# Performance work log

Measured on AMD Instinct MI355X. Metric: run time of the kernel, lower is better.

The kernel has to match this reference:

```python
import jax, jax.numpy as jnp
import numpy as np

C = 128
N = 4096
B = 4
NEG = -9e15


def _bn(x, g, b):
    # training-mode BatchNorm1d over (batch, N); x: [B, C, N]
    mean = x.mean(axis=(0, 2), keepdims=True)
    var = x.var(axis=(0, 2), keepdims=True)  # biased, like torch BN
    xh = (x - mean) * jax.lax.rsqrt(var + 1e-5)
    return xh * g[None, :, None] + b[None, :, None]


def _sa(x, mask2, wqk, wv, bv, wt, bt, g, b):
    # x: [B, C, N]; wqk: [C//4, C] (q and k share weights)
    xq = jnp.einsum('oc,bcn->bno', wqk, x)          # [B, N, C/4]
    xk = jnp.einsum('oc,bcm->bom', wqk, x)          # [B, C/4, N]
    energy = jnp.einsum('bno,bom->bnm', xq, xk)     # [B, N, N]
    energy = jnp.where(mask2, energy, NEG)
    attn = jax.nn.softmax(energy, axis=-1)
    # offset-attention: column-wise L1 renormalization
    attn = attn / (1e-9 + attn.sum(axis=1, keepdims=True))
    xv = jnp.einsum('oc,bcn->bon', wv, x) + bv[None, :, None]
    x_r = jnp.einsum('bcn,bnm->bcm', xv, attn)      # [B, C, N]
    x_r = jax.nn.relu(_bn(jnp.einsum('oc,bcn->bon', wt, x - x_r) + bt[None, :, None], g, b))
    return x + x_r


def setup_inputs() -> dict:
    key = jax.random.key(0)
    ks = jax.random.split(key, 12)
    s = 1.0 / np.sqrt(C)
    return {
        'x': jax.random.normal(ks[0], (B, C, N), jnp.float32),
        'mask': jax.random.randint(ks[1], (B, N), 0, 2, jnp.int32),
        'w1': jax.random.normal(ks[2], (C, C), jnp.float32) * s,
        'g1': jnp.ones((C,), jnp.float32),
        'b1': jnp.zeros((C,), jnp.float32),
        'w2': jax.random.normal(ks[3], (C, C), jnp.float32) * s,
        'g2': jnp.ones((C,), jnp.float32),
        'b2': jnp.zeros((C,), jnp.float32),
        'wqk': jax.random.normal(ks[4], (4, C // 4, C), jnp.float32) * s,
        'wv': jax.random.normal(ks[5], (4, C, C), jnp.float32) * s,
        'bv': jax.random.normal(ks[6], (4, C), jnp.float32) * 0.01,
        'wt': jax.random.normal(ks[7], (4, C, C), jnp.float32) * s,
        'bt': jax.random.normal(ks[8], (4, C), jnp.float32) * 0.01,
        'sg': jnp.ones((4, C), jnp.float32),
        'sb': jnp.zeros((4, C), jnp.float32),
    }


def reference(x, mask, w1, g1, b1, w2, g2, b2, wqk, wv, bv, wt, bt, sg, sb):
    m = mask.astype(bool)
    mask2 = m[:, :, None] & m[:, None, :]           # [B, N, N]
    x = jax.nn.relu(_bn(jnp.einsum('oc,bcn->bon', w1, x), g1, b1))
    x = jax.nn.relu(_bn(jnp.einsum('oc,bcn->bon', w2, x), g2, b2))
    outs = []
    h = x
    for i in range(4):
        h = _sa(h, mask2, wqk[i], wv[i], bv[i], wt[i], bt[i], sg[i], sb[i])
        outs.append(h)
    return jnp.concatenate(outs, axis=1)            # [B, 4C, N]
```

## Files before the change

### kernel.cpp

```cpp
#include <hip/hip_runtime.h>
#include <hip/hip_fp16.h>

constexpr int C = 128;
constexpr int N = 4096;
constexpr int B = 4;

typedef _Float16 f16x8 __attribute__((ext_vector_type(8)));
typedef _Float16 f16x4 __attribute__((ext_vector_type(4)));
typedef float    f32x4 __attribute__((ext_vector_type(4)));

__global__ __launch_bounds__(256) void k_wcvt(const float* __restrict__ w1,
                                              const float* __restrict__ w2,
                                              const float* __restrict__ wv,
                                              const float* __restrict__ wt,
                                              const float* __restrict__ wqk,
                                              _Float16* __restrict__ WF) {
  const int g = blockIdx.x * 256 + threadIdx.x;
  const float* src; int off;
  if (g < 4096)       { src = w1;  off = g; }
  else if (g < 8192)  { src = w2;  off = g - 4096; }
  else if (g < 24576) { src = wv;  off = g - 8192; }
  else if (g < 40960) { src = wt;  off = g - 24576; }
  else                { src = wqk; off = g - 40960; }
  const float4 v = ((const float4*)src)[off];
  f16x4 h = {(_Float16)v.x, (_Float16)v.y, (_Float16)v.z, (_Float16)v.w};
  *(f16x4*)&WF[(size_t)g * 4] = h;
}

__global__ __launch_bounds__(1024) void k_mask(const int* __restrict__ mask,
                                               int* __restrict__ psum,
                                               int* __restrict__ nvb) {
  const int b = blockIdx.x, tid = threadIdx.x;
  __shared__ int wsum[16];
  const int4 mv = *(const int4*)&mask[b * N + tid * 4];
  const int m0 = (mv.x != 0), m1 = (mv.y != 0), m2 = (mv.z != 0), m3 = (mv.w != 0);
  const int s0 = m0, s1 = s0 + m1, s2 = s1 + m2, s3 = s2 + m3;
  const int lane = tid & 63, w = tid >> 6;
  int sc = s3;
#pragma unroll
  for (int o = 1; o < 64; o <<= 1) {
    const int v = __shfl_up(sc, o, 64);
    if (lane >= o) sc += v;
  }
  if (lane == 63) wsum[w] = sc;
  __syncthreads();
  if (tid < 16) {
    int v = wsum[tid];
#pragma unroll
    for (int o = 1; o < 16; o <<= 1) {
      const int u = __shfl_up(v, o, 64);
      if (tid >= o) v += u;
    }
    wsum[tid] = v;
  }
  __syncthreads();
  const int excl = ((w > 0) ? wsum[w - 1] : 0) + sc - s3;
  int4 pv;
  pv.x = excl; pv.y = excl + s0; pv.z = excl + s1; pv.w = excl + s2;
  *(int4*)&psum[b * N + tid * 4] = pv;
  if (tid == 0) nvb[b] = wsum[15];
}

template<bool BIAS, bool STAT, bool F16IN>
__global__ __launch_bounds__(512) void k_gwm(const _Float16* __restrict__ WF,
                                             const void* __restrict__ Xv,
                                             const float* __restrict__ bias,
                                             _Float16* __restrict__ Y,
                                             float* __restrict__ bnpart) {
  __shared__ _Float16 XT[64 * 136];
  __shared__ float statP[4][64], statQ[4][64];
  const int tid = threadIdx.x;
  const int n0 = blockIdx.x * 64, oh = blockIdx.y, b = blockIdx.z;
  if constexpr (F16IN) {
    const _Float16* Xb = (const _Float16*)Xv + (size_t)(b * C) * N + n0;
#pragma unroll
    for (int i = 0; i < 2; i++) {
      const int idx = tid + i * 512;
      const int c = idx >> 3, q = idx & 7;
      const f16x8 v = *(const f16x8*)&Xb[(size_t)c * N + q * 8];
#pragma unroll
      for (int e = 0; e < 8; e++) XT[(q * 8 + e) * 136 + c] = v[e];
    }
  } else {
    const float* Xb = (const float*)Xv + (size_t)(b * C) * N + n0;
#pragma unroll
    for (int i = 0; i < 4; i++) {
      const int idx = tid + i * 512;
      const int c = idx >> 4, q = idx & 15;
      const float4 v = *(const float4*)&Xb[(size_t)c * N + q * 4];
      XT[(q * 4 + 0) * 136 + c] = (_Float16)v.x;
      XT[(q * 4 + 1) * 136 + c] = (_Float16)v.y;
      XT[(q * 4 + 2) * 136 + c] = (_Float16)v.z;
      XT[(q * 4 + 3) * 136 + c] = (_Float16)v.w;
    }
  }
  __syncthreads();
  const int w = tid >> 6, lane = tid & 63, quad = lane >> 4, lr = lane & 15;
  const int nt = w & 3, og = w >> 2;
  const int ob[2] = {oh * 64 + og * 16, oh * 64 + (og + 2) * 16};
  f16x8 aW[2][4];
#pragma unroll
  for (int t = 0; t < 2; t++)
#pragma unroll
    for (int kc = 0; kc < 4; kc++)
      aW[t][kc] = *(const f16x8*)&WF[(size_t)(ob[t] + lr) * 128 + kc * 32 + quad * 8];
  f32x4 acc[2];
  acc[0] = (f32x4){0.f, 0.f, 0.f, 0.f};
  acc[1] = (f32x4){0.f, 0.f, 0.f, 0.f};
#pragma unroll
  for (int kc = 0; kc < 4; kc++) {
    const f16x8 bf = *(const f16x8*)&XT[(nt * 16 + lr) * 136 + kc * 32 + quad * 8];
    acc[0] = __builtin_amdgcn_mfma_f32_16x16x32_f16(aW[0][kc], bf, acc[0], 0, 0, 0);
    acc[1] = __builtin_amdgcn_mfma_f32_16x16x32_f16(aW[1][kc], bf, acc[1], 0, 0, 0);
  }
#pragma unroll
  for (int t = 0; t < 2; t++) {
#pragma unroll
    for (int r = 0; r < 4; r++) {
      const int o = ob[t] + quad * 4 + r;
      const float val = acc[t][r] + (BIAS ? bias[o] : 0.f);
      Y[(size_t)(b * C + o) * N + n0 + nt * 16 + lr] = (_Float16)val;
      if (STAT) {
        float s = val, q = val * val;
        s += __shfl_xor(s, 1, 64); q += __shfl_xor(q, 1, 64);
        s += __shfl_xor(s, 2, 64); q += __shfl_xor(q, 2, 64);
        s += __shfl_xor(s, 4, 64); q += __shfl_xor(q, 4, 64);
        s += __shfl_xor(s, 8, 64); q += __shfl_xor(q, 8, 64);
        if (lr == 0) { statP[nt][o - oh * 64] = s; statQ[nt][o - oh * 64] = q; }
      }
    }
  }
  if (STAT) {
    __syncthreads();
    if (tid < 64) {
      const int o = oh * 64 + tid;
      const float s = statP[0][tid] + statP[1][tid] + statP[2][tid] + statP[3][tid];
      const float q = statQ[0][tid] + statQ[1][tid] + statQ[2][tid] + statQ[3][tid];
      const int part = blockIdx.x * 4 + b;
      bnpart[o * 512 + part] = s;
      bnpart[o * 512 + 256 + part] = q;
    }
  }
}

__global__ __launch_bounds__(256) void k_qv(const _Float16* __restrict__ WFv,
                                            const _Float16* __restrict__ WFqk,
                                            const float* __restrict__ X,
                                            const float* __restrict__ bv,
                                            const int* __restrict__ mask,
                                            const int* __restrict__ psum,
                                            _Float16* __restrict__ XVc,
                                            _Float16* __restrict__ QT,
                                            _Float16* __restrict__ QTc,
                                            float* __restrict__ xvp) {
  __shared__ _Float16 XT[32 * 136];
  __shared__ float SP[2][128];
  const int tid = threadIdx.x;
  const int n0 = blockIdx.x * 32, b = blockIdx.y;
  const float* Xb = X + (size_t)(b * C) * N + n0;
#pragma unroll
  for (int i = 0; i < 4; i++) {
    const int idx = tid + i * 256;
    const int c = idx >> 3, q = idx & 7;
    const float4 v = *(const float4*)&Xb[(size_t)c * N + q * 4];
    XT[(q * 4 + 0) * 136 + c] = (_Float16)v.x;
    XT[(q * 4 + 1) * 136 + c] = (_Float16)v.y;
    XT[(q * 4 + 2) * 136 + c] = (_Float16)v.z;
    XT[(q * 4 + 3) * 136 + c] = (_Float16)v.w;
  }
  __syncthreads();
  const int w = tid >> 6, lane = tid & 63, quad = lane >> 4, lr = lane & 15;
  const int nt = w & 1, og = w >> 1;
  const int n = n0 + nt * 16 + lr;
  const int vld = mask[b * N + n] != 0;
  const int jc = psum[b * N + n];
  f32x4 acc[5];
  const _Float16* Aptr[5];
  int otl[5];
#pragma unroll
  for (int j = 0; j < 5; j++) {
    acc[j] = (f32x4){0.f, 0.f, 0.f, 0.f};
    const int ot = og + 2 * j;
    otl[j] = ot;
    Aptr[j] = (ot < 8) ? (WFv + (size_t)(ot * 16 + lr) * 128)
                       : (WFqk + (size_t)((ot - 8) * 16 + lr) * 128);
  }
#pragma unroll
  for (int kc = 0; kc < 4; kc++) {
    const f16x8 bf = *(const f16x8*)&XT[(nt * 16 + lr) * 136 + kc * 32 + quad * 8];
#pragma unroll
    for (int j = 0; j < 5; j++) {
      const f16x8 a = *(const f16x8*)&Aptr[j][kc * 32 + quad * 8];
      acc[j] = __builtin_amdgcn_mfma_f32_16x16x32_f16(a, bf, acc[j], 0, 0, 0);
    }
  }
#pragma unroll
  for (int j = 0; j < 5; j++) {
    const int ot = otl[j];
    if (ot < 8) {
      float v[4];
#pragma unroll
      for (int r = 0; r < 4; r++) v[r] = acc[j][r] + bv[ot * 16 + quad * 4 + r];
      if (vld) {
#pragma unroll
        for (int r = 0; r < 4; r++)
          XVc[(size_t)(b * C + ot * 16 + quad * 4 + r) * N + jc] = (_Float16)v[r];
      }
      float s[4];
#pragma unroll
      for (int r = 0; r < 4; r++) s[r] = vld ? 0.f : v[r];
#pragma unroll
      for (int o = 1; o <= 8; o <<= 1) {
#pragma unroll
        for (int r = 0; r < 4; r++) s[r] += __shfl_xor(s[r], o, 64);
      }
      if (lr == 0) {
#pragma unroll
        for (int r = 0; r < 4; r++) SP[nt][ot * 16 + quad * 4 + r] = s[r];
      }
    } else {
      f16x4 qv;
#pragma unroll
      for (int r = 0; r < 4; r++) qv[r] = (_Float16)acc[j][r];
      const int qo = (ot - 8) * 16 + quad * 4;
      *(f16x4*)&QT[((size_t)b * N + n) * 32 + qo] = qv;
      if (vld) *(f16x4*)&QTc[((size_t)b * N + jc) * 32 + qo] = qv;
    }
  }
  __syncthreads();
  if (tid < 128)
    xvp[(size_t)(b * C + tid) * 128 + blockIdx.x] = SP[0][tid] + SP[1][tid];
}

__global__ __launch_bounds__(512) void k_sm(const _Float16* __restrict__ QTc,
                                            const int* __restrict__ nvb,
                                            const float* __restrict__ xvp,
                                            float* __restrict__ xvi,
                                            float2* __restrict__ rowst) {
  const int b = blockIdx.y, tid = threadIdx.x;
  if (blockIdx.x == 256) {
    __shared__ float xr[128][4];
    const int c = tid >> 2, q = tid & 3;
    const float* src = xvp + (size_t)(b * C + c) * 128 + q * 32;
    float v = 0.f;
#pragma unroll
    for (int i = 0; i < 32; i++) v += src[i];
    xr[c][q] = v;
    __syncthreads();
    if (tid < 128) xvi[b * C + tid] = xr[tid][0] + xr[tid][1] + xr[tid][2] + xr[tid][3];
    return;
  }
  const int Nv = nvb[b];
  const int NvpB = (Nv + 63) & ~63;
  const int n0 = blockIdx.x * 16;
  if (n0 >= NvpB) return;
  __shared__ float redM[8][16], redS[8][16];
  const _Float16* Qb = QTc + (size_t)b * N * 32;
  const int w = tid >> 6, lane = tid & 63, quad = lane >> 4, lr = lane & 15;
  const f16x8 aF = *(const f16x8*)&Qb[(size_t)(n0 + lr) * 32 + quad * 8];
  float mx[4] = {-3e38f, -3e38f, -3e38f, -3e38f};
  float s[4] = {0.f, 0.f, 0.f, 0.f};
  for (int ms = 0; ms < NvpB; ms += 128) {
    const int mrow = ms + w * 16 + lr;
    const f16x8 bF = *(const f16x8*)&Qb[(size_t)mrow * 32 + quad * 8];
    f32x4 d = (f32x4){0.f, 0.f, 0.f, 0.f};
    d = __builtin_amdgcn_mfma_f32_16x16x32_f16(aF, bF, d, 0, 0, 0);
    const float bias = (mrow < Nv) ? 0.0f : -1e30f;
#pragma unroll
    for (int r = 0; r < 4; r++) {
      const float dv = d[r] + bias;
      if (dv > mx[r]) {
        s[r] *= __expf(mx[r] - dv);
        mx[r] = dv;
      }
      s[r] += __expf(dv - mx[r]);
    }
  }
#pragma unroll
  for (int r = 0; r < 4; r++) {
#pragma unroll
    for (int o = 1; o <= 8; o <<= 1) {
      const float mo = __shfl_xor(mx[r], o, 64);
      const float so = __shfl_xor(s[r], o, 64);
      const float mn = fmaxf(mx[r], mo);
      s[r] = s[r] * __expf(mx[r] - mn) + so * __expf(mo - mn);
      mx[r] = mn;
    }
  }
  if (lr == 0)
#pragma unroll
    for (int r = 0; r < 4; r++) {
      redM[w][quad * 4 + r] = mx[r];
      redS[w][quad * 4 + r] = s[r];
    }
  __syncthreads();
  if (tid < 16) {
    float M = redM[0][tid];
#pragma unroll
    for (int k = 1; k < 8; k++) M = fmaxf(M, redM[k][tid]);
    float tot = 0.f;
#pragma unroll
    for (int k = 0; k < 8; k++) tot += redS[k][tid] * __expf(redM[k][tid] - M);
    const int row = n0 + tid;
    const bool valid = row < Nv;
    float2 rv;
    rv.x = valid ? M : 1e30f;
    rv.y = valid ? (1.0f / tot) : 0.0f;
    rowst[b * N + row] = rv;
  }
}

__global__ __launch_bounds__(512, 4) void k_pv(const _Float16* __restrict__ QT,
                                               const _Float16* __restrict__ QTc,
                                               const _Float16* __restrict__ XVc,
                                               const float* __restrict__ H,
                                               const int* __restrict__ mask,
                                               const float2* __restrict__ rowst,
                                               const int* __restrict__ nvb,
                                               const float* __restrict__ xvi,
                                               _Float16* __restrict__ Td) {
  __shared__ _Float16 XVs[2][128 * 72];
  __shared__ _Float16 PsT[2][32 * 72];
  __shared__ float colPart[4][32];
  __shared__ float colS[32];
  const int tid = threadIdx.x;
  const int m0 = blockIdx.x * 32, b = blockIdx.y;
  const int Nv = nvb[b];
  const int ns = ((Nv + 63) & ~63) >> 6;
  const _Float16* Qa = QT + (size_t)b * N * 32;
  const _Float16* Qc = QTc + (size_t)b * N * 32;
  const _Float16* XVb = XVc + (size_t)(b * C) * N;
  const float2* rsB = rowst + (size_t)b * N;
  const int w = tid >> 6, lane = tid & 63, quad = lane >> 4, lr = lane & 15;
  const int msub = w & 1, nsub = w >> 1;
  const f16x8 bGm = *(const f16x8*)&Qa[(size_t)(m0 + msub * 16 + lr) * 32 + quad * 8];
  const float vmb =
      (mask[b * N + m0 + msub * 16 + lr] != 0) ? 0.0f : -1e30f;
  const int sc0 = tid >> 3, sh0 = tid & 7;
  const int sc1 = sc0 + 64;
  f32x4 acc[2];
  acc[0] = (f32x4){0.f, 0.f, 0.f, 0.f};
  acc[1] = (f32x4){0.f, 0.f, 0.f, 0.f};
  float cs = 0.f;

  auto produce = [&](int k0, int bf) {
    const f16x8 aGn = *(const f16x8*)&Qc[(size_t)(k0 + nsub * 16 + lr) * 32 + quad * 8];
    const f16x8 xv0 = *(const f16x8*)&XVb[(size_t)sc0 * N + k0 + sh0 * 8];
    const f16x8 xv1 = *(const f16x8*)&XVb[(size_t)sc1 * N + k0 + sh0 * 8];
    const int nb = k0 + nsub * 16 + quad * 4;
    const float4 r01 = *(const float4*)&rsB[nb];
    const float4 r23 = *(const float4*)&rsB[nb + 2];
    f32x4 e = (f32x4){0.f, 0.f, 0.f, 0.f};
    e = __builtin_amdgcn_mfma_f32_16x16x32_f16(aGn, bGm, e, 0, 0, 0);
    *(f16x8*)&XVs[bf][sc0 * 72 + sh0 * 8] = xv0;
    *(f16x8*)&XVs[bf][sc1 * 72 + sh0 * 8] = xv1;
    const float p0 = __expf(e[0] - r01.x + vmb) * r01.y;
    const float p1 = __expf(e[1] - r01.z + vmb) * r01.w;
    const float p2 = __expf(e[2] - r23.x + vmb) * r23.y;
    const float p3 = __expf(e[3] - r23.z + vmb) * r23.w;
    cs += (p0 + p1) + (p2 + p3);
    f16x4 pp = {(_Float16)p0, (_Float16)p1, (_Float16)p2, (_Float16)p3};
    *(f16x4*)&PsT[bf][(msub * 16 + lr) * 72 + nsub * 16 + quad * 4] = pp;
  };
  auto consume = [&](int bf) {
    const int c0 = w * 16;
    const f16x8 a0 = *(const f16x8*)&XVs[bf][(c0 + lr) * 72 + quad * 8];
    const f16x8 a1 = *(const f16x8*)&XVs[bf][(c0 + lr) * 72 + 32 + quad * 8];
    const f16x8 b00 = *(const f16x8*)&PsT[bf][lr * 72 + quad * 8];
    const f16x8 b01 = *(const f16x8*)&PsT[bf][lr * 72 + 32 + quad * 8];
    const f16x8 b10 = *(const f16x8*)&PsT[bf][(16 + lr) * 72 + quad * 8];
    const f16x8 b11 = *(const f16x8*)&PsT[bf][(16 + lr) * 72 + 32 + quad * 8];
    acc[0] = __builtin_amdgcn_mfma_f32_16x16x32_f16(a0, b00, acc[0], 0, 0, 0);
    acc[0] = __builtin_amdgcn_mfma_f32_16x16x32_f16(a1, b01, acc[0], 0, 0, 0);
    acc[1] = __builtin_amdgcn_mfma_f32_16x16x32_f16(a0, b10, acc[1], 0, 0, 0);
    acc[1] = __builtin_amdgcn_mfma_f32_16x16x32_f16(a1, b11, acc[1], 0, 0, 0);
  };

  if (ns > 0) produce(0, 0);
  __syncthreads();
  for (int it = 0; it < ns; it += 2) {
    if (it + 1 < ns) produce((it + 1) * 64, 1);
    consume(0);
    __syncthreads();
    if (it + 1 < ns) {
      if (it + 2 < ns) produce((it + 2) * 64, 0);
      consume(1);
      __syncthreads();
    }
  }
  cs += __shfl_xor(cs, 16, 64);
  cs += __shfl_xor(cs, 32, 64);
  if (quad == 0) colPart[nsub][msub * 16 + lr] = cs;
  __syncthreads();
  if (tid < 32)
    colS[tid] = colPart[0][tid] + colPart[1][tid] + colPart[2][tid] + colPart[3][tid];
  __syncthreads();
  const float ninvq = (float)(N - Nv) * 0.000244140625f;
  const float rdiv0 = 1.0f / (1e-9f + colS[lr] + ninvq);
  const float rdiv1 = 1.0f / (1e-9f + colS[16 + lr] + ninvq);
  const int cg = b * C + w * 16 + quad * 4;
#pragma unroll
  for (int r = 0; r < 4; r++) {
    const float xadd = xvi[cg + r] * 0.000244140625f;
    const size_t gi0 = (size_t)(cg + r) * N + m0 + lr;
    Td[gi0] = (_Float16)(H[gi0] - (acc[0][r] + xadd) * rdiv0);
    const size_t gi1 = (size_t)(cg + r) * N + m0 + 16 + lr;
    Td[gi1] = (_Float16)(H[gi1] - (acc[1][r] + xadd) * rdiv1);
  }
}

template<bool RES>
__global__ __launch_bounds__(256) void k_apply(const _Float16* __restrict__ T2,
                                               const float* __restrict__ bnpart,
                                               const float* __restrict__ gamma,
                                               const float* __restrict__ beta,
                                               float* __restrict__ H,
                                               float* __restrict__ Out) {
  __shared__ float rs[4], rq[4], bc[2];
  const int tid = threadIdx.x;
  const int f = (blockIdx.x * 256 + tid) * 4;
  const int c = (blockIdx.x >> 2) & 127;
  float s = bnpart[c * 512 + tid];
  float q = bnpart[c * 512 + 256 + tid];
#pragma unroll
  for (int o = 1; o <= 32; o <<= 1) { s += __shfl_xor(s, o, 64); q += __shfl_xor(q, o, 64); }
  if ((tid & 63) == 0) { rs[tid >> 6] = s; rq[tid >> 6] = q; }
  __syncthreads();
  if (tid == 0) {
    const float st = rs[0] + rs[1] + rs[2] + rs[3];
    const float qt = rq[0] + rq[1] + rq[2] + rq[3];
    const float inv = 1.0f / (B * N);
    const float mean = st * inv;
    const float var = qt * inv - mean * mean;
    const float sc = gamma[c] * rsqrtf(var + 1e-5f);
    bc[0] = sc;
    bc[1] = beta[c] - mean * sc;
  }
  __syncthreads();
  const float sc = bc[0], sh = bc[1];
  const f16x4 t = *(const f16x4*)&T2[f];
  float4 r;
  r.x = fmaxf((float)t[0] * sc + sh, 0.f);
  r.y = fmaxf((float)t[1] * sc + sh, 0.f);
  r.z = fmaxf((float)t[2] * sc + sh, 0.f);
  r.w = fmaxf((float)t[3] * sc + sh, 0.f);
  if (RES) {
    const float4 h = *(const float4*)&H[f];
    r.x += h.x; r.y += h.y; r.z += h.z; r.w += h.w;
    *(float4*)&H[f] = r;
    const int b = f >> 19;
    const int rem = f & (C * N - 1);
    *(float4*)&Out[(size_t)b * (4 * C * N) + rem] = r;
  } else {
    *(float4*)&H[f] = r;
  }
}

extern "C" void kernel_launch(void* const* d_in, const int* in_sizes, int n_in,
                              void* d_out, int out_size, void* d_ws, size_t ws_size,
                              hipStream_t stream) {
  const float* x    = (const float*)d_in[0];
  const int*   mask = (const int*)  d_in[1];
  const float* w1   = (const float*)d_in[2];
  const float* g1   = (const float*)d_in[3];
  const float* b1   = (const float*)d_in[4];
  const float* w2   = (const float*)d_in[5];
  const float* g2   = (const float*)d_in[6];
  const float* b2   = (const float*)d_in[7];
  const float* wqk  = (const float*)d_in[8];
  const float* wv   = (const float*)d_in[9];
  const float* bv   = (const float*)d_in[10];
  const float* wt   = (const float*)d_in[11];
  const float* bt   = (const float*)d_in[12];
  const float* sg   = (const float*)d_in[13];
  const float* sb   = (const float*)d_in[14];
  float* out = (float*)d_out;

  char* p = (char*)d_ws;
  auto alloc = [&](size_t bytes) { char* r = p; p += (bytes + 255) & ~(size_t)255; return r; };
  float*    H      = (float*)   alloc((size_t)B * C * N * 4);
  _Float16* T2h    = (_Float16*)alloc((size_t)B * C * N * 2);
  _Float16* Td16   = (_Float16*)alloc((size_t)B * C * N * 2);
  _Float16* QT     = (_Float16*)alloc((size_t)B * N * 32 * 2);
  _Float16* QTc    = (_Float16*)alloc((size_t)B * N * 32 * 2);
  _Float16* XVc    = (_Float16*)alloc((size_t)B * C * N * 2);
  float2*   rowst  = (float2*)  alloc((size_t)B * N * 8);
  float*    bnpart = (float*)   alloc((size_t)C * 512 * 4);
  int*      psum   = (int*)     alloc((size_t)B * N * 4);
  int*      nvb    = (int*)     alloc(256);
  float*    xvp    = (float*)   alloc((size_t)B * C * 128 * 4);
  float*    xvi    = (float*)   alloc((size_t)B * C * 4);
  _Float16* WF     = (_Float16*)alloc((size_t)180224 * 2);
  (void)ws_size;
  _Float16* wf1  = WF;
  _Float16* wf2  = WF + 16384;
  _Float16* wfv  = WF + 32768;
  _Float16* wft  = WF + 98304;
  _Float16* wfqk = WF + 163840;

  k_wcvt<<<176, 256, 0, stream>>>(w1, w2, wv, wt, wqk, WF);
  k_mask<<<B, 1024, 0, stream>>>(mask, psum, nvb);
  hipMemsetAsync(QTc, 0, (size_t)B * N * 32 * 2 + (size_t)B * C * N * 2, stream);

  k_gwm<false, true, false><<<dim3(64, 2, B), 512, 0, stream>>>(wf1, x, nullptr, T2h, bnpart);
  k_apply<false><<<2048, 256, 0, stream>>>(T2h, bnpart, g1, b1, H, nullptr);
  k_gwm<false, true, false><<<dim3(64, 2, B), 512, 0, stream>>>(wf2, H, nullptr, T2h, bnpart);
  k_apply<false><<<2048, 256, 0, stream>>>(T2h, bnpart, g2, b2, H, nullptr);

  for (int L = 0; L < 4; L++) {
    k_qv<<<dim3(128, B), 256, 0, stream>>>(wfv + (size_t)L * 16384, wfqk + (size_t)L * 4096,
                                           H, bv + L * C, mask, psum, XVc, QT, QTc, xvp);
    k_sm<<<dim3(257, B), 512, 0, stream>>>(QTc, nvb, xvp, xvi, rowst);
    k_pv<<<dim3(128, B), 512, 0, stream>>>(QT, QTc, XVc, H, mask, rowst, nvb, xvi, Td16);
    k_gwm<true, true, true><<<dim3(64, 2, B), 512, 0, stream>>>(wft + (size_t)L * 16384, Td16, bt + L * C, T2h, bnpart);
    k_apply<true><<<2048, 256, 0, stream>>>(T2h, bnpart, sg + L * C, sb + L * C, H, out + (size_t)L * C * N);
  }
}
```

Measured before the change: 438.8 us.

## Fuse trans-conv GEMM and BN partial stats into the PV attention kernel

The attention-output kernel now stages the (H - x_r) tile in shared memory and multiplies it by the trans-conv weights with MFMA inside the same kernel. It writes T2h and per-block BN partial sums directly, which removes the separate k_gwm launch and the Td16 round trip through global memory. The bnpart layout grows to 512 partials per channel, and k_apply is templated to reduce either 256 or 512 partials. The cost is extra per-block work and reuse of the XVs shared buffer for the tile. Each block also reads the whole weight matrix from global memory.

```diff
diff --git a/kernel.cpp b/kernel.cpp
--- a/kernel.cpp
+++ b/kernel.cpp
@@ -137,8 +137,8 @@
       const float s = statP[0][tid] + statP[1][tid] + statP[2][tid] + statP[3][tid];
       const float q = statQ[0][tid] + statQ[1][tid] + statQ[2][tid] + statQ[3][tid];
       const int part = blockIdx.x * 4 + b;
-      bnpart[o * 512 + part] = s;
-      bnpart[o * 512 + 256 + part] = q;
+      bnpart[o * 1024 + part] = s;
+      bnpart[o * 1024 + 512 + part] = q;
     }
   }
 }
@@ -313,12 +313,15 @@
 __global__ __launch_bounds__(512, 4) void k_pv(const _Float16* __restrict__ QT,
                                                const _Float16* __restrict__ QTc,
                                                const _Float16* __restrict__ XVc,
+                                               const _Float16* __restrict__ WFt,
                                                const float* __restrict__ H,
                                                const int* __restrict__ mask,
                                                const float2* __restrict__ rowst,
                                                const int* __restrict__ nvb,
                                                const float* __restrict__ xvi,
-                                               _Float16* __restrict__ Td) {
+                                               const float* __restrict__ bt,
+                                               _Float16* __restrict__ T2h,
+                                               float* __restrict__ bnpart) {
   __shared__ _Float16 XVs[2][128 * 72];
   __shared__ _Float16 PsT[2][32 * 72];
   __shared__ float colPart[4][32];
@@ -398,18 +401,55 @@
   const float ninvq = (float)(N - Nv) * 0.000244140625f;
   const float rdiv0 = 1.0f / (1e-9f + colS[lr] + ninvq);
   const float rdiv1 = 1.0f / (1e-9f + colS[16 + lr] + ninvq);
-  const int cg = b * C + w * 16 + quad * 4;
+  const int cg = w * 16 + quad * 4;
+  _Float16* TdS = &XVs[0][0];
+  {
+    f16x4 t0, t1;
+#pragma unroll
+    for (int r = 0; r < 4; r++) {
+      const float xadd = xvi[b * C + cg + r] * 0.000244140625f;
+      const size_t gi0 = (size_t)(b * C + cg + r) * N + m0 + lr;
+      const size_t gi1 = gi0 + 16;
+      t0[r] = (_Float16)(H[gi0] - (acc[0][r] + xadd) * rdiv0);
+      t1[r] = (_Float16)(H[gi1] - (acc[1][r] + xadd) * rdiv1);
+    }
+    *(f16x4*)&TdS[lr * 136 + cg] = t0;
+    *(f16x4*)&TdS[(16 + lr) * 136 + cg] = t1;
+  }
+  __syncthreads();
+  f32x4 acc2[2];
+  acc2[0] = (f32x4){0.f, 0.f, 0.f, 0.f};
+  acc2[1] = (f32x4){0.f, 0.f, 0.f, 0.f};
+#pragma unroll
+  for (int kc = 0; kc < 4; kc++) {
+    const f16x8 aT = *(const f16x8*)&WFt[(size_t)(w * 16 + lr) * 128 + kc * 32 + quad * 8];
+    const f16x8 bT0 = *(const f16x8*)&TdS[lr * 136 + kc * 32 + quad * 8];
+    const f16x8 bT1 = *(const f16x8*)&TdS[(16 + lr) * 136 + kc * 32 + quad * 8];
+    acc2[0] = __builtin_amdgcn_mfma_f32_16x16x32_f16(aT, bT0, acc2[0], 0, 0, 0);
+    acc2[1] = __builtin_amdgcn_mfma_f32_16x16x32_f16(aT, bT1, acc2[1], 0, 0, 0);
+  }
+  const int oo = w * 16 + quad * 4;
+  const int part = b * 128 + blockIdx.x;
 #pragma unroll
   for (int r = 0; r < 4; r++) {
-    const float xadd = xvi[cg + r] * 0.000244140625f;
-    const size_t gi0 = (size_t)(cg + r) * N + m0 + lr;
-    Td[gi0] = (_Float16)(H[gi0] - (acc[0][r] + xadd) * rdiv0);
-    const size_t gi1 = (size_t)(cg + r) * N + m0 + 16 + lr;
-    Td[gi1] = (_Float16)(H[gi1] - (acc[1][r] + xadd) * rdiv1);
-  }
-}
-
-template<bool RES>
+    const float v0 = acc2[0][r] + bt[oo + r];
+    const float v1 = acc2[1][r] + bt[oo + r];
+    const size_t go = (size_t)(b * C + oo + r) * N + m0 + lr;
+    T2h[go] = (_Float16)v0;
+    T2h[go + 16] = (_Float16)v1;
+    float s = v0 + v1, q = v0 * v0 + v1 * v1;
+    s += __shfl_xor(s, 1, 64); q += __shfl_xor(q, 1, 64);
+    s += __shfl_xor(s, 2, 64); q += __shfl_xor(q, 2, 64);
+    s += __shfl_xor(s, 4, 64); q += __shfl_xor(q, 4, 64);
+    s += __shfl_xor(s, 8, 64); q += __shfl_xor(q, 8, 64);
+    if (lr == 0) {
+      bnpart[(oo + r) * 1024 + part] = s;
+      bnpart[(oo + r) * 1024 + 512 + part] = q;
+    }
+  }
+}
+
+template<bool RES, int PARTS>
 __global__ __launch_bounds__(256) void k_apply(const _Float16* __restrict__ T2,
                                                const float* __restrict__ bnpart,
                                                const float* __restrict__ gamma,
@@ -420,8 +460,14 @@
   const int tid = threadIdx.x;
   const int f = (blockIdx.x * 256 + tid) * 4;
   const int c = (blockIdx.x >> 2) & 127;
-  float s = bnpart[c * 512 + tid];
-  float q = bnpart[c * 512 + 256 + tid];
+  float s, q;
+  if (PARTS == 512) {
+    s = bnpart[c * 1024 + tid] + bnpart[c * 1024 + 256 + tid];
+    q = bnpart[c * 1024 + 512 + tid] + bnpart[c * 1024 + 768 + tid];
+  } else {
+    s = bnpart[c * 1024 + tid];
+    q = bnpart[c * 1024 + 512 + tid];
+  }
 #pragma unroll
   for (int o = 1; o <= 32; o <<= 1) { s += __shfl_xor(s, o, 64); q += __shfl_xor(q, o, 64); }
   if ((tid & 63) == 0) { rs[tid >> 6] = s; rq[tid >> 6] = q; }
@@ -480,12 +526,11 @@
   auto alloc = [&](size_t bytes) { char* r = p; p += (bytes + 255) & ~(size_t)255; return r; };
   float*    H      = (float*)   alloc((size_t)B * C * N * 4);
   _Float16* T2h    = (_Float16*)alloc((size_t)B * C * N * 2);
-  _Float16* Td16   = (_Float16*)alloc((size_t)B * C * N * 2);
   _Float16* QT     = (_Float16*)alloc((size_t)B * N * 32 * 2);
   _Float16* QTc    = (_Float16*)alloc((size_t)B * N * 32 * 2);
   _Float16* XVc    = (_Float16*)alloc((size_t)B * C * N * 2);
   float2*   rowst  = (float2*)  alloc((size_t)B * N * 8);
-  float*    bnpart = (float*)   alloc((size_t)C * 512 * 4);
+  float*    bnpart = (float*)   alloc((size_t)C * 1024 * 4);
   int*      psum   = (int*)     alloc((size_t)B * N * 4);
   int*      nvb    = (int*)     alloc(256);
   float*    xvp    = (float*)   alloc((size_t)B * C * 128 * 4);
@@ -503,16 +548,17 @@
   hipMemsetAsync(QTc, 0, (size_t)B * N * 32 * 2 + (size_t)B * C * N * 2, stream);
 
   k_gwm<false, true, false><<<dim3(64, 2, B), 512, 0, stream>>>(wf1, x, nullptr, T2h, bnpart);
-  k_apply<false><<<2048, 256, 0, stream>>>(T2h, bnpart, g1, b1, H, nullptr);
+  k_apply<false, 256><<<2048, 256, 0, stream>>>(T2h, bnpart, g1, b1, H, nullptr);
   k_gwm<false, true, false><<<dim3(64, 2, B), 512, 0, stream>>>(wf2, H, nullptr, T2h, bnpart);
-  k_apply<false><<<2048, 256, 0, stream>>>(T2h, bnpart, g2, b2, H, nullptr);
+  k_apply<false, 256><<<2048, 256, 0, stream>>>(T2h, bnpart, g2, b2, H, nullptr);
 
   for (int L = 0; L < 4; L++) {
     k_qv<<<dim3(128, B), 256, 0, stream>>>(wfv + (size_t)L * 16384, wfqk + (size_t)L * 4096,
                                            H, bv + L * C, mask, psum, XVc, QT, QTc, xvp);
     k_sm<<<dim3(257, B), 512, 0, stream>>>(QTc, nvb, xvp, xvi, rowst);
-    k_pv<<<dim3(128, B), 512, 0, stream>>>(QT, QTc, XVc, H, mask, rowst, nvb, xvi, Td16);
-    k_gwm<true, true, true><<<dim3(64, 2, B), 512, 0, stream>>>(wft + (size_t)L * 16384, Td16, bt + L * C, T2h, bnpart);
-    k_apply<true><<<2048, 256, 0, stream>>>(T2h, bnpart, sg + L * C, sb + L * C, H, out + (size_t)L * C * N);
-  }
-}
+    k_pv<<<dim3(128, B), 512, 0, stream>>>(QT, QTc, XVc, wft + (size_t)L * 16384, H, mask,
+                                           rowst, nvb, xvi, bt + L * C, T2h, bnpart);
+    k_apply<true, 512><<<2048, 256, 0, stream>>>(T2h, bnpart, sg + L * C, sb + L * C, H,
+                                                 out + (size_t)L * C * N);
+  }
+}
```

After: 412.6 us, median of 2. -6.0%, faster.
